# Kernel optimization log

Measured on AMD Instinct MI355X. Metric: run time of the kernel, lower is better.

The kernel has to match this reference:

```python
import jax, jax.numpy as jnp
import numpy as np
import math

DIM = 512
B, L = 32, 2048
NEG = jnp.float32(-2**32 + 1)  # padding value used by the torch module

def setup_inputs() -> dict:
    key = jax.random.key(0)
    k1, k2, k3, k4 = jax.random.split(key, 4)
    Ez = jax.random.normal(k1, (B, L, DIM), dtype=jnp.float32)
    # 6 Linear(dim, dim, bias=False) layers each for Q, K, V; weight is [out, in]
    s = 1.0 / math.sqrt(DIM)
    Wq = jax.random.uniform(k2, (6, DIM, DIM), dtype=jnp.float32, minval=-s, maxval=s)
    Wk = jax.random.uniform(k3, (6, DIM, DIM), dtype=jnp.float32, minval=-s, maxval=s)
    Wv = jax.random.uniform(k4, (6, DIM, DIM), dtype=jnp.float32, minval=-s, maxval=s)
    return {"Ez": Ez, "Wq": Wq, "Wk": Wk, "Wv": Wv, "z": 3}

def reference(Ez, Wq, Wk, Wv, z):
    dim = Ez.shape[-1]
    # nn.Linear: x @ W.T
    q = jnp.einsum('bld,ed->ble', Ez, Wq[z])
    k = jnp.einsum('bld,ed->ble', Ez, Wk[z])
    v = jnp.einsum('bld,ed->ble', Ez, Wv[z])
    scores = jnp.einsum('bqe,bke->bqk', q, k) / jnp.float32(math.sqrt(dim))
    Lq = scores.shape[-1]
    tril = jnp.tril(jnp.ones((Lq, Lq), dtype=jnp.float32))  # causal mask
    scores = jnp.where(tril[None, :, :] == 0, NEG, scores)
    attn = jax.nn.softmax(scores, axis=-1)
    return jnp.einsum('bqk,bke->bqe', attn, v)
```

## Files before the change

kernel.cpp:

```cpp
#include <hip/hip_runtime.h>
#include <hip/hip_bf16.h>


typedef __attribute__((ext_vector_type(8))) short short8;
typedef __attribute__((ext_vector_type(4))) short short4v;
typedef __attribute__((ext_vector_type(4))) float f32x4;

#define DIM 512
#define LSEQ 2048
#define NB 32
#define SCALE 0.04419417382415922f
#define LOG2E 1.4426950408889634f

__device__ __forceinline__ short f2bs(float f) {
  __hip_bfloat16 h = __float2bfloat16(f);
  return __builtin_bit_cast(short, h);
}

__device__ __forceinline__ void gld16(const void* g, void* l) {
  __builtin_amdgcn_global_load_lds(
      (const unsigned int __attribute__((address_space(1)))*)g,
      (unsigned int __attribute__((address_space(3)))*)l, 16, 0, 0);
}

__global__ __launch_bounds__(256) void wcvt_kernel(
    const float* __restrict__ Wq, const float* __restrict__ Wk,
    const float* __restrict__ Wv, const int* __restrict__ zp,
    short* __restrict__ Wb) {
  int z = *zp;
  int i = blockIdx.x * 256 + threadIdx.x;
  int g = i >> 15;
  int off = (i & 32767) * 8;
  int n = off >> 9, d0 = off & 511;
  int kt = d0 >> 5, c = d0 & 31;
  int sw = ((c >> 3) ^ ((n >> 1) & 3));
  const float* src = (g == 0 ? Wq : (g == 1 ? Wk : Wv)) + (size_t)z * DIM * DIM + off;
  float4 a = *(const float4*)src, b = *(const float4*)(src + 4);
  short8 v;
  v[0]=f2bs(a.x); v[1]=f2bs(a.y); v[2]=f2bs(a.z); v[3]=f2bs(a.w);
  v[4]=f2bs(b.x); v[5]=f2bs(b.y); v[6]=f2bs(b.z); v[7]=f2bs(b.w);
  *(short8*)&Wb[((size_t)(g * 16 + kt) * 512 + n) * 32 + sw * 8] = v;
}

__global__ __launch_bounds__(512, 4) void proj_kernel(
    const float* __restrict__ Ez, const short* __restrict__ Wb,
    short* __restrict__ Qb, short* __restrict__ Kb, short* __restrict__ Vtb) {
  int g = blockIdx.z;
  const short* W = Wb + (size_t)g * 16 * 512 * 32;
  __shared__ short As[2][64 * 32];
  __shared__ short Bs[2][512 * 32];
  int tid = threadIdx.x, lane = tid & 63, wid = tid >> 6;
  int l15 = lane & 15, lg = lane >> 4;
  int m0 = blockIdx.x * 64;
  int sw = (l15 >> 1) & 3;
  f32x4 zero4 = {0.f, 0.f, 0.f, 0.f};
  f32x4 acc[4][4];
  #pragma unroll
  for (int mi = 0; mi < 4; mi++)
    #pragma unroll
    for (int ni = 0; ni < 4; ni++) acc[mi][ni] = zero4;

  int arow = tid >> 3, aq = tid & 7;
  int aoff = arow * 32 + (((aq >> 1) ^ ((arow >> 1) & 3)) << 3) + (aq & 1) * 4;
  const float* aptr = Ez + (size_t)(m0 + arow) * DIM + aq * 4;

  {
    float4 a = *(const float4*)aptr;
    short4v av;
    av[0]=f2bs(a.x); av[1]=f2bs(a.y); av[2]=f2bs(a.z); av[3]=f2bs(a.w);
    *(short4v*)&As[0][aoff] = av;
    #pragma unroll
    for (int ii = 0; ii < 4; ii++) {
      int s = wid * 4 + ii;
      gld16(W + s * 512 + lane * 8, &Bs[0][s * 512]);
    }
  }
  __syncthreads();

  #pragma unroll 2
  for (int kt = 0; kt < 16; kt++) {
    int cur = kt & 1;
    float4 a;
    if (kt < 15) {
      a = *(const float4*)(aptr + (kt + 1) * 32);
      #pragma unroll
      for (int ii = 0; ii < 4; ii++) {
        int s = wid * 4 + ii;
        gld16(W + (size_t)(kt + 1) * 16384 + s * 512 + lane * 8, &Bs[cur ^ 1][s * 512]);
      }
    }
    short8 af[4], bf[4];
    #pragma unroll
    for (int mi = 0; mi < 4; mi++)
      af[mi] = *(const short8*)&As[cur][(mi * 16 + l15) * 32 + ((lg ^ sw) << 3)];
    #pragma unroll
    for (int ni = 0; ni < 4; ni++)
      bf[ni] = *(const short8*)&Bs[cur][(wid * 64 + ni * 16 + l15) * 32 + ((lg ^ sw) << 3)];
    __builtin_amdgcn_s_setprio(1);
    #pragma unroll
    for (int mi = 0; mi < 4; mi++)
      #pragma unroll
      for (int ni = 0; ni < 4; ni++)
        acc[mi][ni] = __builtin_amdgcn_mfma_f32_16x16x32_bf16(af[mi], bf[ni], acc[mi][ni], 0, 0, 0);
    __builtin_amdgcn_s_setprio(0);
    if (kt < 15) {
      short4v av;
      av[0]=f2bs(a.x); av[1]=f2bs(a.y); av[2]=f2bs(a.z); av[3]=f2bs(a.w);
      *(short4v*)&As[cur ^ 1][aoff] = av;
    }
    __syncthreads();
  }

  if (g == 2) {
    #pragma unroll
    for (int mi = 0; mi < 4; mi++) {
      int gm0 = m0 + mi * 16 + lg * 4;
      int b = gm0 >> 11, l0 = gm0 & (LSEQ - 1);
      int t = l0 >> 5, c0 = l0 & 31;
      #pragma unroll
      for (int ni = 0; ni < 4; ni++) {
        int e = wid * 64 + ni * 16 + l15;
        short4v v;
        v[0]=f2bs(acc[mi][ni][0]); v[1]=f2bs(acc[mi][ni][1]);
        v[2]=f2bs(acc[mi][ni][2]); v[3]=f2bs(acc[mi][ni][3]);
        size_t idx = ((size_t)(b * 64 + t) * 512 + e) * 32
                     + (((c0 >> 3) ^ ((e >> 1) & 3)) << 3) + (c0 & 7);
        *(short4v*)&Vtb[idx] = v;
      }
    }
  } else {
    short* dst = (g == 0 ? Qb : Kb);
    float sc = (g == 0 ? SCALE * LOG2E : 1.0f);
    #pragma unroll
    for (int mi = 0; mi < 4; mi++) {
      int gm0 = m0 + mi * 16 + lg * 4;
      #pragma unroll
      for (int ni = 0; ni < 4; ni++) {
        int gn = wid * 64 + ni * 16 + l15;
        #pragma unroll
        for (int r = 0; r < 4; r++)
          dst[(size_t)(gm0 + r) * DIM + gn] = f2bs(acc[mi][ni][r] * sc);
      }
    }
  }
}

__device__ __forceinline__ void stage_kv(const short* __restrict__ Kb,
                                         const short* __restrict__ Vtb,
                                         short* Klbuf, short* Vlbuf,
                                         int batch, int t, int wid, int lane) {
  #pragma unroll
  for (int ii = 0; ii < 4; ii++) {
    int r = wid + ii * 8;
    const short* src = Kb + (size_t)(batch * LSEQ + t * 32 + r) * DIM + ((lane ^ wid) * 8);
    gld16(src, Klbuf + r * 512);
  }
  const short* vt = Vtb + (size_t)(batch * 64 + t) * 16384;
  #pragma unroll
  for (int ii = 0; ii < 4; ii++) {
    int s = wid * 4 + ii;
    gld16(vt + s * 512 + lane * 8, Vlbuf + s * 512);
  }
}

__global__ __launch_bounds__(512, 2) void attn_kernel(
    const short* __restrict__ Qb, const short* __restrict__ Kb,
    const short* __restrict__ Vtb, float* __restrict__ out) {
  __shared__ short Kl[2][32 * 512];
  __shared__ short Vl[2][512 * 32];
  __shared__ short P_lds[8][16][40];
  int tid = threadIdx.x, lane = tid & 63, wid = tid >> 6;
  int l15 = lane & 15, lg = lane >> 4;
  int batch = blockIdx.x;
  f32x4 zero4 = {0.f, 0.f, 0.f, 0.f};
  short8 ones;
  #pragma unroll
  for (int i = 0; i < 8; i++) ones[i] = (short)0x3F80;

  int a0 = (l15 >> 2) & 1, b0 = l15 & 3;
  int kqE = l15 * 512 + 8 * (lg ^ b0) + 32 * a0;
  int kqO = l15 * 512 + 8 * (lg ^ b0) - 32 * a0;
  int voff = l15 * 32 + 8 * (lg ^ ((l15 >> 1) & 3));
  short* pw = &P_lds[wid][lg * 4][l15];
  const short* pr = &P_lds[wid][l15][lg * 8];

  for (int qpass = 0; qpass < 2; qpass++) {
    int qt = qpass ? (int)blockIdx.y : 15 - (int)blockIdx.y;
    int qb0 = qt * 128;
    int q0w = qb0 + wid * 16;
    int nt = qt * 4 + 4;

    stage_kv(Kb, Vtb, Kl[0], Vl[0], batch, 0, wid, lane);

    const short* qrow = Qb + (size_t)(batch * LSEQ + q0w + l15) * DIM;
    short8 qf[16];
    #pragma unroll
    for (int kt = 0; kt < 16; kt++) qf[kt] = *(const short8*)(qrow + kt * 32 + lg * 8);

    f32x4 oacc[32];
    #pragma unroll
    for (int i = 0; i < 32; i++) oacc[i] = zero4;
    f32x4 dacc = zero4;
    float mrun = -1e30f;

    __syncthreads();

    for (int t = 0; t < nt; t++) {
      int cur = t & 1;
      if (t + 1 < nt)
        stage_kv(Kb, Vtb, Kl[cur ^ 1], Vl[cur ^ 1], batch, t + 1, wid, lane);

      if (t * 32 <= q0w + 15) {
        const short* pE = Kl[cur] + kqE;
        const short* pO = Kl[cur] + kqO;
        f32x4 sacc[2] = {zero4, zero4};
        __builtin_amdgcn_s_setprio(1);
        #pragma unroll
        for (int kt = 0; kt < 16; kt += 2) {
          short8 k0 = *(const short8*)(pE + 32 * kt);
          short8 k1 = *(const short8*)(pE + 8192 + 32 * kt);
          sacc[0] = __builtin_amdgcn_mfma_f32_16x16x32_bf16(qf[kt], k0, sacc[0], 0, 0, 0);
          sacc[1] = __builtin_amdgcn_mfma_f32_16x16x32_bf16(qf[kt], k1, sacc[1], 0, 0, 0);
          short8 k2 = *(const short8*)(pO + 32 * (kt + 1));
          short8 k3 = *(const short8*)(pO + 8192 + 32 * (kt + 1));
          sacc[0] = __builtin_amdgcn_mfma_f32_16x16x32_bf16(qf[kt + 1], k2, sacc[0], 0, 0, 0);
          sacc[1] = __builtin_amdgcn_mfma_f32_16x16x32_bf16(qf[kt + 1], k3, sacc[1], 0, 0, 0);
        }
        __builtin_amdgcn_s_setprio(0);
        float s0[4], s1[4];
        if (t * 32 + 31 > q0w) {
          #pragma unroll
          for (int r = 0; r < 4; r++) {
            int q = q0w + lg * 4 + r;
            s0[r] = (t * 32 + l15 > q) ? -1e30f : sacc[0][r];
            s1[r] = (t * 32 + 16 + l15 > q) ? -1e30f : sacc[1][r];
          }
        } else {
          #pragma unroll
          for (int r = 0; r < 4; r++) { s0[r] = sacc[0][r]; s1[r] = sacc[1][r]; }
        }
        float lm = fmaxf(fmaxf(fmaxf(s0[0], s0[1]), fmaxf(s0[2], s0[3])),
                         fmaxf(fmaxf(s1[0], s1[1]), fmaxf(s1[2], s1[3])));
        if (__any(lm > mrun + 11.5f)) {
          float mx = lm;
          #pragma unroll
          for (int off = 1; off < 64; off <<= 1) mx = fmaxf(mx, __shfl_xor(mx, off, 64));
          float alpha = exp2f(mrun - mx);
          mrun = mx;
          dacc[0] *= alpha; dacc[1] *= alpha; dacc[2] *= alpha; dacc[3] *= alpha;
          #pragma unroll
          for (int et = 0; et < 32; et++) {
            oacc[et][0] *= alpha; oacc[et][1] *= alpha;
            oacc[et][2] *= alpha; oacc[et][3] *= alpha;
          }
        }
        #pragma unroll
        for (int r = 0; r < 4; r++) {
          pw[r * 40] = f2bs(exp2f(s0[r] - mrun));
          pw[r * 40 + 16] = f2bs(exp2f(s1[r] - mrun));
        }
        short8 pa = *(const short8*)pr;
        const short* vb = Vl[cur] + voff;
        __builtin_amdgcn_s_setprio(1);
        dacc = __builtin_amdgcn_mfma_f32_16x16x32_bf16(pa, ones, dacc, 0, 0, 0);
        #pragma unroll
        for (int et = 0; et < 32; et++) {
          short8 bv = *(const short8*)(vb + et * 512);
          oacc[et] = __builtin_amdgcn_mfma_f32_16x16x32_bf16(pa, bv, oacc[et], 0, 0, 0);
        }
        __builtin_amdgcn_s_setprio(0);
      }
      __syncthreads();
    }
    float inv[4];
    #pragma unroll
    for (int r = 0; r < 4; r++) inv[r] = 1.0f / dacc[r];
    #pragma unroll
    for (int et = 0; et < 32; et++)
      #pragma unroll
      for (int r = 0; r < 4; r++) {
        int q = q0w + lg * 4 + r;
        out[((size_t)(batch * LSEQ + q)) * DIM + et * 16 + l15] = oacc[et][r] * inv[r];
      }
  }
}

extern "C" void kernel_launch(void* const* d_in, const int* in_sizes, int n_in,
                              void* d_out, int out_size, void* d_ws, size_t ws_size,
                              hipStream_t stream) {
  const float* Ez = (const float*)d_in[0];
  const float* Wq = (const float*)d_in[1];
  const float* Wk = (const float*)d_in[2];
  const float* Wv = (const float*)d_in[3];
  const int* zp = (const int*)d_in[4];
  float* out = (float*)d_out;
  short* Qb = (short*)d_ws;
  short* Kb = Qb + (size_t)NB * LSEQ * DIM;
  short* Vtb = Kb + (size_t)NB * LSEQ * DIM;
  short* Wb = (short*)d_out;
  hipLaunchKernelGGL(wcvt_kernel, dim3(384), dim3(256), 0, stream,
                     Wq, Wk, Wv, zp, Wb);
  hipLaunchKernelGGL(proj_kernel, dim3(1024, 1, 3), dim3(512), 0, stream,
                     Ez, Wb, Qb, Kb, Vtb);
  hipLaunchKernelGGL(attn_kernel, dim3(32, 8), dim3(512), 0, stream,
                     Qb, Kb, Vtb, out);
}
```

Before: 436.5 us.

## Load first quarter of V tile directly from global into registers, shrinking V LDS

```diff
diff --git a/kernel.cpp b/kernel.cpp
--- a/kernel.cpp
+++ b/kernel.cpp
@@ -123,8 +123,10 @@
         short4v v;
         v[0]=f2bs(acc[mi][ni][0]); v[1]=f2bs(acc[mi][ni][1]);
         v[2]=f2bs(acc[mi][ni][2]); v[3]=f2bs(acc[mi][ni][3]);
-        size_t idx = ((size_t)(b * 64 + t) * 512 + e) * 32
-                     + (((c0 >> 3) ^ ((e >> 1) & 3)) << 3) + (c0 & 7);
+        size_t base = ((size_t)(b * 64 + t) * 512 + e) * 32;
+        size_t idx = (wid < 2)
+            ? (base + c0)
+            : (base + (((c0 >> 3) ^ ((e >> 1) & 3)) << 3) + (c0 & 7));
         *(short4v*)&Vtb[idx] = v;
       }
     }
@@ -157,9 +159,9 @@
   }
   const short* vt = Vtb + (size_t)(batch * 64 + t) * 16384;
   #pragma unroll
-  for (int ii = 0; ii < 4; ii++) {
-    int s = wid * 4 + ii;
-    gld16(vt + s * 512 + lane * 8, Vlbuf + s * 512);
+  for (int ii = 0; ii < 3; ii++) {
+    int s = wid * 3 + ii;
+    gld16(vt + (8 + s) * 512 + lane * 8, Vlbuf + s * 512);
   }
 }
 
@@ -167,7 +169,7 @@
     const short* __restrict__ Qb, const short* __restrict__ Kb,
     const short* __restrict__ Vtb, float* __restrict__ out) {
   __shared__ short Kl[2][32 * 512];
-  __shared__ short Vl[2][512 * 32];
+  __shared__ short Vl[2][384 * 32];
   __shared__ short P_lds[8][16][40];
   int tid = threadIdx.x, lane = tid & 63, wid = tid >> 6;
   int l15 = lane & 15, lg = lane >> 4;
@@ -181,6 +183,7 @@
   int kqE = l15 * 512 + 8 * (lg ^ b0) + 32 * a0;
   int kqO = l15 * 512 + 8 * (lg ^ b0) - 32 * a0;
   int voff = l15 * 32 + 8 * (lg ^ ((l15 >> 1) & 3));
+  int vgo = l15 * 32 + lg * 8;
   short* pw = &P_lds[wid][lg * 4][l15];
   const short* pr = &P_lds[wid][l15][lg * 8];
 
@@ -211,6 +214,11 @@
         stage_kv(Kb, Vtb, Kl[cur ^ 1], Vl[cur ^ 1], batch, t + 1, wid, lane);
 
       if (t * 32 <= q0w + 15) {
+        short8 bvr[8];
+        const short* vt = Vtb + (size_t)(batch * 64 + t) * 16384;
+        #pragma unroll
+        for (int et = 0; et < 8; et++)
+          bvr[et] = *(const short8*)(vt + et * 512 + vgo);
         const short* pE = Kl[cur] + kqE;
         const short* pO = Kl[cur] + kqO;
         f32x4 sacc[2] = {zero4, zero4};
@@ -227,20 +235,17 @@
           sacc[1] = __builtin_amdgcn_mfma_f32_16x16x32_bf16(qf[kt + 1], k3, sacc[1], 0, 0, 0);
         }
         __builtin_amdgcn_s_setprio(0);
-        float s0[4], s1[4];
         if (t * 32 + 31 > q0w) {
           #pragma unroll
           for (int r = 0; r < 4; r++) {
             int q = q0w + lg * 4 + r;
-            s0[r] = (t * 32 + l15 > q) ? -1e30f : sacc[0][r];
-            s1[r] = (t * 32 + 16 + l15 > q) ? -1e30f : sacc[1][r];
+            if (t * 32 + l15 > q) sacc[0][r] = -1e30f;
+            if (t * 32 + 16 + l15 > q) sacc[1][r] = -1e30f;
           }
-        } else {
-          #pragma unroll
-          for (int r = 0; r < 4; r++) { s0[r] = sacc[0][r]; s1[r] = sacc[1][r]; }
-        }
-        float lm = fmaxf(fmaxf(fmaxf(s0[0], s0[1]), fmaxf(s0[2], s0[3])),
-                         fmaxf(fmaxf(s1[0], s1[1]), fmaxf(s1[2], s1[3])));
+        }
+        float lm = fmaxf(
+            fmaxf(fmaxf(sacc[0][0], sacc[0][1]), fmaxf(sacc[0][2], sacc[0][3])),
+            fmaxf(fmaxf(sacc[1][0], sacc[1][1]), fmaxf(sacc[1][2], sacc[1][3])));
         if (__any(lm > mrun + 11.5f)) {
           float mx = lm;
           #pragma unroll
@@ -256,16 +261,19 @@
         }
         #pragma unroll
         for (int r = 0; r < 4; r++) {
-          pw[r * 40] = f2bs(exp2f(s0[r] - mrun));
-          pw[r * 40 + 16] = f2bs(exp2f(s1[r] - mrun));
+          pw[r * 40] = f2bs(exp2f(sacc[0][r] - mrun));
+          pw[r * 40 + 16] = f2bs(exp2f(sacc[1][r] - mrun));
         }
         short8 pa = *(const short8*)pr;
         const short* vb = Vl[cur] + voff;
         __builtin_amdgcn_s_setprio(1);
         dacc = __builtin_amdgcn_mfma_f32_16x16x32_bf16(pa, ones, dacc, 0, 0, 0);
         #pragma unroll
-        for (int et = 0; et < 32; et++) {
-          short8 bv = *(const short8*)(vb + et * 512);
+        for (int et = 0; et < 8; et++)
+          oacc[et] = __builtin_amdgcn_mfma_f32_16x16x32_bf16(pa, bvr[et], oacc[et], 0, 0, 0);
+        #pragma unroll
+        for (int et = 8; et < 32; et++) {
+          short8 bv = *(const short8*)(vb + (et - 8) * 512);
           oacc[et] = __builtin_amdgcn_mfma_f32_16x16x32_bf16(pa, bv, oacc[et], 0, 0, 0);
         }
         __builtin_amdgcn_s_setprio(0);
```

After: 571.6 us. 31.0% more time.

## Software-pipeline PV of previous tile with QK of current tile

Applied to the files above, without the earlier changes.

```diff
diff --git a/kernel.cpp b/kernel.cpp
--- a/kernel.cpp
+++ b/kernel.cpp
@@ -145,16 +145,19 @@
   }
 }
 
-__device__ __forceinline__ void stage_kv(const short* __restrict__ Kb,
-                                         const short* __restrict__ Vtb,
-                                         short* Klbuf, short* Vlbuf,
-                                         int batch, int t, int wid, int lane) {
+__device__ __forceinline__ void stage_k(const short* __restrict__ Kb,
+                                        short* Klbuf,
+                                        int batch, int t, int wid, int lane) {
   #pragma unroll
   for (int ii = 0; ii < 4; ii++) {
     int r = wid + ii * 8;
     const short* src = Kb + (size_t)(batch * LSEQ + t * 32 + r) * DIM + ((lane ^ wid) * 8);
     gld16(src, Klbuf + r * 512);
   }
+}
+__device__ __forceinline__ void stage_v(const short* __restrict__ Vtb,
+                                        short* Vlbuf,
+                                        int batch, int t, int wid, int lane) {
   const short* vt = Vtb + (size_t)(batch * 64 + t) * 16384;
   #pragma unroll
   for (int ii = 0; ii < 4; ii++) {
@@ -190,7 +193,7 @@
     int q0w = qb0 + wid * 16;
     int nt = qt * 4 + 4;
 
-    stage_kv(Kb, Vtb, Kl[0], Vl[0], batch, 0, wid, lane);
+    stage_k(Kb, Kl[0], batch, 0, wid, lane);
 
     const short* qrow = Qb + (size_t)(batch * LSEQ + q0w + l15) * DIM;
     short8 qf[16];
@@ -202,18 +205,48 @@
     for (int i = 0; i < 32; i++) oacc[i] = zero4;
     f32x4 dacc = zero4;
     float mrun = -1e30f;
+    short8 pa;
 
     __syncthreads();
 
     for (int t = 0; t < nt; t++) {
       int cur = t & 1;
       if (t + 1 < nt)
-        stage_kv(Kb, Vtb, Kl[cur ^ 1], Vl[cur ^ 1], batch, t + 1, wid, lane);
-
-      if (t * 32 <= q0w + 15) {
+        stage_k(Kb, Kl[cur ^ 1], batch, t + 1, wid, lane);
+      stage_v(Vtb, Vl[cur], batch, t, wid, lane);
+
+      bool act = (t * 32 <= q0w + 15);
+      bool actp = (t > 0) && ((t - 1) * 32 <= q0w + 15);
+      f32x4 sacc[2] = {zero4, zero4};
+      if (act && actp) {
         const short* pE = Kl[cur] + kqE;
         const short* pO = Kl[cur] + kqO;
-        f32x4 sacc[2] = {zero4, zero4};
+        const short* vb = Vl[cur ^ 1] + voff;
+        __builtin_amdgcn_s_setprio(1);
+        dacc = __builtin_amdgcn_mfma_f32_16x16x32_bf16(pa, ones, dacc, 0, 0, 0);
+        #pragma unroll
+        for (int kt = 0; kt < 16; kt += 2) {
+          short8 k0 = *(const short8*)(pE + 32 * kt);
+          short8 k1 = *(const short8*)(pE + 8192 + 32 * kt);
+          sacc[0] = __builtin_amdgcn_mfma_f32_16x16x32_bf16(qf[kt], k0, sacc[0], 0, 0, 0);
+          sacc[1] = __builtin_amdgcn_mfma_f32_16x16x32_bf16(qf[kt], k1, sacc[1], 0, 0, 0);
+          short8 v0 = *(const short8*)(vb + (kt * 2) * 512);
+          short8 v1 = *(const short8*)(vb + (kt * 2 + 1) * 512);
+          oacc[kt * 2] = __builtin_amdgcn_mfma_f32_16x16x32_bf16(pa, v0, oacc[kt * 2], 0, 0, 0);
+          oacc[kt * 2 + 1] = __builtin_amdgcn_mfma_f32_16x16x32_bf16(pa, v1, oacc[kt * 2 + 1], 0, 0, 0);
+          short8 k2 = *(const short8*)(pO + 32 * (kt + 1));
+          short8 k3 = *(const short8*)(pO + 8192 + 32 * (kt + 1));
+          sacc[0] = __builtin_amdgcn_mfma_f32_16x16x32_bf16(qf[kt + 1], k2, sacc[0], 0, 0, 0);
+          sacc[1] = __builtin_amdgcn_mfma_f32_16x16x32_bf16(qf[kt + 1], k3, sacc[1], 0, 0, 0);
+          short8 v2 = *(const short8*)(vb + (kt * 2 + 2) * 512);
+          short8 v3 = *(const short8*)(vb + (kt * 2 + 3) * 512);
+          oacc[kt * 2 + 2] = __builtin_amdgcn_mfma_f32_16x16x32_bf16(pa, v2, oacc[kt * 2 + 2], 0, 0, 0);
+          oacc[kt * 2 + 3] = __builtin_amdgcn_mfma_f32_16x16x32_bf16(pa, v3, oacc[kt * 2 + 3], 0, 0, 0);
+        }
+        __builtin_amdgcn_s_setprio(0);
+      } else if (act) {
+        const short* pE = Kl[cur] + kqE;
+        const short* pO = Kl[cur] + kqO;
         __builtin_amdgcn_s_setprio(1);
         #pragma unroll
         for (int kt = 0; kt < 16; kt += 2) {
@@ -227,20 +260,29 @@
           sacc[1] = __builtin_amdgcn_mfma_f32_16x16x32_bf16(qf[kt + 1], k3, sacc[1], 0, 0, 0);
         }
         __builtin_amdgcn_s_setprio(0);
-        float s0[4], s1[4];
+      } else if (actp) {
+        const short* vb = Vl[cur ^ 1] + voff;
+        __builtin_amdgcn_s_setprio(1);
+        dacc = __builtin_amdgcn_mfma_f32_16x16x32_bf16(pa, ones, dacc, 0, 0, 0);
+        #pragma unroll
+        for (int et = 0; et < 32; et++) {
+          short8 bv = *(const short8*)(vb + et * 512);
+          oacc[et] = __builtin_amdgcn_mfma_f32_16x16x32_bf16(pa, bv, oacc[et], 0, 0, 0);
+        }
+        __builtin_amdgcn_s_setprio(0);
+      }
+      if (act) {
         if (t * 32 + 31 > q0w) {
           #pragma unroll
           for (int r = 0; r < 4; r++) {
             int q = q0w + lg * 4 + r;
-            s0[r] = (t * 32 + l15 > q) ? -1e30f : sacc[0][r];
-            s1[r] = (t * 32 + 16 + l15 > q) ? -1e30f : sacc[1][r];
+            if (t * 32 + l15 > q) sacc[0][r] = -1e30f;
+            if (t * 32 + 16 + l15 > q) sacc[1][r] = -1e30f;
           }
-        } else {
-          #pragma unroll
-          for (int r = 0; r < 4; r++) { s0[r] = sacc[0][r]; s1[r] = sacc[1][r]; }
-        }
-        float lm = fmaxf(fmaxf(fmaxf(s0[0], s0[1]), fmaxf(s0[2], s0[3])),
-                         fmaxf(fmaxf(s1[0], s1[1]), fmaxf(s1[2], s1[3])));
+        }
+        float lm = fmaxf(
+            fmaxf(fmaxf(sacc[0][0], sacc[0][1]), fmaxf(sacc[0][2], sacc[0][3])),
+            fmaxf(fmaxf(sacc[1][0], sacc[1][1]), fmaxf(sacc[1][2], sacc[1][3])));
         if (__any(lm > mrun + 11.5f)) {
           float mx = lm;
           #pragma unroll
@@ -256,21 +298,21 @@
         }
         #pragma unroll
         for (int r = 0; r < 4; r++) {
-          pw[r * 40] = f2bs(exp2f(s0[r] - mrun));
-          pw[r * 40 + 16] = f2bs(exp2f(s1[r] - mrun));
-        }
-        short8 pa = *(const short8*)pr;
-        const short* vb = Vl[cur] + voff;
-        __builtin_amdgcn_s_setprio(1);
-        dacc = __builtin_amdgcn_mfma_f32_16x16x32_bf16(pa, ones, dacc, 0, 0, 0);
-        #pragma unroll
-        for (int et = 0; et < 32; et++) {
-          short8 bv = *(const short8*)(vb + et * 512);
-          oacc[et] = __builtin_amdgcn_mfma_f32_16x16x32_bf16(pa, bv, oacc[et], 0, 0, 0);
-        }
-        __builtin_amdgcn_s_setprio(0);
+          pw[r * 40] = f2bs(exp2f(sacc[0][r] - mrun));
+          pw[r * 40 + 16] = f2bs(exp2f(sacc[1][r] - mrun));
+        }
+        pa = *(const short8*)pr;
       }
       __syncthreads();
+    }
+    if ((nt - 1) * 32 <= q0w + 15) {
+      const short* vb = Vl[(nt - 1) & 1] + voff;
+      dacc = __builtin_amdgcn_mfma_f32_16x16x32_bf16(pa, ones, dacc, 0, 0, 0);
+      #pragma unroll
+      for (int et = 0; et < 32; et++) {
+        short8 bv = *(const short8*)(vb + et * 512);
+        oacc[et] = __builtin_amdgcn_mfma_f32_16x16x32_bf16(pa, bv, oacc[et], 0, 0, 0);
+      }
     }
     float inv[4];
     #pragma unroll
@@ -282,6 +324,7 @@
         int q = q0w + lg * 4 + r;
         out[((size_t)(batch * LSEQ + q)) * DIM + et * 16 + l15] = oacc[et][r] * inv[r];
       }
+    __syncthreads();
   }
 }
 
```

Result: faster. 420.0 us (-3.8%).
